# Kernel optimization log

Measured on AMD Instinct MI355X. Metric: run time of the kernel, lower is better.

## Reference

```python
import jax, jax.numpy as jnp
import numpy as np

E, K, B = 64, 8, 32
IN_DIM, OUT_DIM = 1024, 1024


def setup_inputs() -> dict:
    key = jax.random.key(0)
    k1, k2, k3, k4, k5, k6 = jax.random.split(key, 6)
    return {
        "weight_probs": jax.random.uniform(k1, (B, K), dtype=jnp.float32),
        "bias_probs": jax.random.uniform(k2, (B, K), dtype=jnp.float32),
        "weight_indices": jax.random.randint(k3, (B, K), 0, E, dtype=jnp.int64),
        "bias_indices": jax.random.randint(k4, (B, K), 0, E, dtype=jnp.int64),
        # parameter banks: one linear layer's params per expert
        "weight_bank": jax.random.normal(k5, (E, OUT_DIM, IN_DIM), dtype=jnp.float32) * 0.02,
        "bias_bank": jax.random.normal(k6, (E, OUT_DIM), dtype=jnp.float32) * 0.02,
    }


def reference(weight_probs, bias_probs, weight_indices, bias_indices, weight_bank, bias_bank):
    # _select_parameters: gather per-(batch, top_k) expert params
    sel_w = weight_bank[weight_indices]          # [B, K, O, I]
    sel_b = bias_bank[bias_indices]              # [B, K, O]
    # _compute_mixture: probability-weighted sum over the top_k axis
    weight_mixture = jnp.einsum("bk,bkoi->boi", weight_probs, sel_w)  # [B, O, I]
    bias_mixture = jnp.einsum("bk,bko->bo", bias_probs, sel_b)        # [B, O]
    return weight_mixture, bias_mixture
```

## Files before the change

kernel.cpp:

```cpp
#include <hip/hip_runtime.h>
#include <hip/hip_bf16.h>


typedef __attribute__((ext_vector_type(8)))  short short8v;
typedef __attribute__((ext_vector_type(16))) float f32x16;

constexpr int E = 64;
constexpr int K = 8;
constexpr int B = 32;
constexpr int IN_DIM = 1024;
constexpr int OUT_DIM = 1024;

constexpr int    NCOL     = OUT_DIM * IN_DIM;
constexpr int    BLK      = 256;
constexpr int    GRID     = 1024;
constexpr int    WAVES    = GRID * 4;
constexpr int    CGROUPS  = NCOL / 32;
constexpr int    STEPS    = CGROUPS / WAVES;
constexpr int    WM_ELEMS = B * NCOL;
constexpr int    OB4      = OUT_DIM / 4;
constexpr size_t WS_NEEDED = 2 * 4 * 64 * 8 * sizeof(short);

__global__ void ParameterMixture_build_afrag(
    const float* __restrict__ wprobs,
    const int*   __restrict__ widx,
    short*       __restrict__ afrag)
{
    const int t    = threadIdx.x;
    const int s    = t >> 6;
    const int lane = t & 63;
    const int m    = lane & 31;
    const int kh   = (lane >> 5) * 8;

#pragma unroll
    for (int j = 0; j < 8; ++j) {
        const int e = s * 16 + kh + j;
        float p = 0.f;
#pragma unroll
        for (int k2 = 0; k2 < K; ++k2)
            p += (widx[m * K + k2] == e) ? wprobs[m * K + k2] : 0.f;
        const __hip_bfloat16 h  = __float2bfloat16(p);
        const float          hf = __bfloat162float(h);
        const __hip_bfloat16 l  = __float2bfloat16(p - hf);
        afrag[(0 * 4 + s) * 512 + lane * 8 + j] = __builtin_bit_cast(short, h);
        afrag[(1 * 4 + s) * 512 + lane * 8 + j] = __builtin_bit_cast(short, l);
    }
}

__global__ __launch_bounds__(BLK, 4) void ParameterMixture_86835648790543_kernel(
    const float* __restrict__ wbank,
    const short* __restrict__ afrag,
    const float* __restrict__ bprobs,
    const int*   __restrict__ bidx,
    const float* __restrict__ bbank,
    float*       __restrict__ out)
{
    const int bid  = blockIdx.x;
    const int t    = threadIdx.x;
    const int wv   = t >> 6;
    const int lane = t & 63;

    if (bid < 32) {
        const int tt   = bid * BLK + t;
        const int b    = tt / OB4;
        const int off4 = tt % OB4;
        const float4* __restrict__ bb4 = (const float4*)bbank;
        float4 a4 = make_float4(0.f, 0.f, 0.f, 0.f);
#pragma unroll
        for (int k = 0; k < K; ++k) {
            const float p = bprobs[b * K + k];
            const int   e = bidx[b * K + k];
            const float4 v = bb4[e * OB4 + off4];
            a4.x += p * v.x; a4.y += p * v.y;
            a4.z += p * v.z; a4.w += p * v.w;
        }
        ((float4*)(out + WM_ELEMS))[tt] = a4;
    }

    short8v aH[4], aL[4];
#pragma unroll
    for (int s = 0; s < 4; ++s) {
        aH[s] = *(const short8v*)(afrag + s * 512 + lane * 8);
        aL[s] = *(const short8v*)(afrag + 2048 + s * 512 + lane * 8);
    }

    const int    cl   = lane & 31;
    const int    kh   = (lane >> 5) * 8;
    const size_t ncol = (size_t)NCOL;

    for (int step = 0; step < STEPS; ++step) {
        const int col0 = ((bid * 4 + wv) + step * WAVES) * 32;
        const float* __restrict__ wcol = wbank + col0 + cl;

        float w[4][8];
#pragma unroll
        for (int s = 0; s < 4; ++s)
#pragma unroll
            for (int j = 0; j < 8; ++j)
                w[s][j] = wcol[(size_t)(s * 16 + kh + j) * ncol];

        f32x16 acc;
#pragma unroll
        for (int i = 0; i < 16; ++i) acc[i] = 0.f;

#pragma unroll
        for (int s = 0; s < 4; ++s) {
            short8v bh, bl;
#pragma unroll
            for (int j = 0; j < 8; ++j) {
                const float x = w[s][j];
                const __hip_bfloat16 h  = __float2bfloat16(x);
                const float          hf = __bfloat162float(h);
                const __hip_bfloat16 l  = __float2bfloat16(x - hf);
                bh[j] = __builtin_bit_cast(short, h);
                bl[j] = __builtin_bit_cast(short, l);
            }
            acc = __builtin_amdgcn_mfma_f32_32x32x16_bf16(aH[s], bh, acc, 0, 0, 0);
            acc = __builtin_amdgcn_mfma_f32_32x32x16_bf16(aH[s], bl, acc, 0, 0, 0);
            acc = __builtin_amdgcn_mfma_f32_32x32x16_bf16(aL[s], bh, acc, 0, 0, 0);
        }

        float* __restrict__ ob = out + (size_t)((lane >> 5) * 4) * ncol + col0 + cl;
#pragma unroll
        for (int reg = 0; reg < 16; ++reg) {
            const int row = (reg & 3) + 8 * (reg >> 2);
            ob[(size_t)row * ncol] = acc[reg];
        }
    }
}

extern "C" void kernel_launch(void* const* d_in, const int* in_sizes, int n_in,
                              void* d_out, int out_size, void* d_ws, size_t ws_size,
                              hipStream_t stream) {
    const float* wprobs = (const float*)d_in[0];
    const float* bprobs = (const float*)d_in[1];
    const int*   widx   = (const int*)d_in[2];
    const int*   bidx   = (const int*)d_in[3];
    const float* wbank  = (const float*)d_in[4];
    const float* bbank  = (const float*)d_in[5];
    float*       out    = (float*)d_out;

    short* afrag = (short*)d_ws;

    ParameterMixture_build_afrag<<<1, BLK, 0, stream>>>(wprobs, widx, afrag);
    ParameterMixture_86835648790543_kernel<<<GRID, BLK, 0, stream>>>(
        wbank, afrag, bprobs, bidx, bbank, out);
}
```

Measured before the change: 93.83 us.

## Fuse A-fragment build into main kernel, contiguous column ranges, nontemporal stores

Drops the separate single-block kernel that built the bf16 hi/lo probability fragments. Each wave now rebuilds them in registers from the routing probabilities, which removes one launch and the dependency between kernels at the cost of redundant per-wave ALU work. Each wave now walks a contiguous range of columns instead of strided ones, and the loop is marked not to unroll. Output stores use nontemporal hints to avoid polluting the cache with the large write-once result.

```diff
diff --git a/kernel.cpp b/kernel.cpp
--- a/kernel.cpp
+++ b/kernel.cpp
@@ -11,47 +11,20 @@
 constexpr int IN_DIM = 1024;
 constexpr int OUT_DIM = 1024;
 
-constexpr int    NCOL     = OUT_DIM * IN_DIM;
-constexpr int    BLK      = 256;
-constexpr int    GRID     = 1024;
-constexpr int    WAVES    = GRID * 4;
-constexpr int    CGROUPS  = NCOL / 32;
-constexpr int    STEPS    = CGROUPS / WAVES;
-constexpr int    WM_ELEMS = B * NCOL;
-constexpr int    OB4      = OUT_DIM / 4;
-constexpr size_t WS_NEEDED = 2 * 4 * 64 * 8 * sizeof(short);
-
-__global__ void ParameterMixture_build_afrag(
-    const float* __restrict__ wprobs,
-    const int*   __restrict__ widx,
-    short*       __restrict__ afrag)
-{
-    const int t    = threadIdx.x;
-    const int s    = t >> 6;
-    const int lane = t & 63;
-    const int m    = lane & 31;
-    const int kh   = (lane >> 5) * 8;
-
-#pragma unroll
-    for (int j = 0; j < 8; ++j) {
-        const int e = s * 16 + kh + j;
-        float p = 0.f;
-#pragma unroll
-        for (int k2 = 0; k2 < K; ++k2)
-            p += (widx[m * K + k2] == e) ? wprobs[m * K + k2] : 0.f;
-        const __hip_bfloat16 h  = __float2bfloat16(p);
-        const float          hf = __bfloat162float(h);
-        const __hip_bfloat16 l  = __float2bfloat16(p - hf);
-        afrag[(0 * 4 + s) * 512 + lane * 8 + j] = __builtin_bit_cast(short, h);
-        afrag[(1 * 4 + s) * 512 + lane * 8 + j] = __builtin_bit_cast(short, l);
-    }
-}
+constexpr int NCOL     = OUT_DIM * IN_DIM;
+constexpr int BLK      = 256;
+constexpr int GRID     = 1024;
+constexpr int WAVES    = GRID * 4;
+constexpr int STEPS    = NCOL / 32 / WAVES;
+constexpr int WM_ELEMS = B * NCOL;
+constexpr int OB4      = OUT_DIM / 4;
 
 __global__ __launch_bounds__(BLK, 4) void ParameterMixture_86835648790543_kernel(
+    const float* __restrict__ wprobs,
+    const float* __restrict__ bprobs,
+    const int*   __restrict__ widx,
+    const int*   __restrict__ bidx,
     const float* __restrict__ wbank,
-    const short* __restrict__ afrag,
-    const float* __restrict__ bprobs,
-    const int*   __restrict__ bidx,
     const float* __restrict__ bbank,
     float*       __restrict__ out)
 {
@@ -59,6 +32,9 @@
     const int t    = threadIdx.x;
     const int wv   = t >> 6;
     const int lane = t & 63;
+    const int m    = lane & 31;
+    const int kh   = (lane >> 5) * 8;
+    const int cl   = lane & 31;
 
     if (bid < 32) {
         const int tt   = bid * BLK + t;
@@ -77,19 +53,37 @@
         ((float4*)(out + WM_ELEMS))[tt] = a4;
     }
 
+    float wp[K];
+    int   wi[K];
+#pragma unroll
+    for (int k2 = 0; k2 < K; ++k2) {
+        wp[k2] = wprobs[m * K + k2];
+        wi[k2] = widx[m * K + k2];
+    }
     short8v aH[4], aL[4];
 #pragma unroll
     for (int s = 0; s < 4; ++s) {
-        aH[s] = *(const short8v*)(afrag + s * 512 + lane * 8);
-        aL[s] = *(const short8v*)(afrag + 2048 + s * 512 + lane * 8);
+#pragma unroll
+        for (int j = 0; j < 8; ++j) {
+            const int e = s * 16 + kh + j;
+            float p = 0.f;
+#pragma unroll
+            for (int k2 = 0; k2 < K; ++k2)
+                p += (wi[k2] == e) ? wp[k2] : 0.f;
+            const __hip_bfloat16 h  = __float2bfloat16(p);
+            const float          hf = __bfloat162float(h);
+            const __hip_bfloat16 l  = __float2bfloat16(p - hf);
+            aH[s][j] = __builtin_bit_cast(short, h);
+            aL[s][j] = __builtin_bit_cast(short, l);
+        }
     }
 
-    const int    cl   = lane & 31;
-    const int    kh   = (lane >> 5) * 8;
-    const size_t ncol = (size_t)NCOL;
+    const size_t ncol    = (size_t)NCOL;
+    const int    wave_id = bid * 4 + wv;
 
+#pragma unroll 1
     for (int step = 0; step < STEPS; ++step) {
-        const int col0 = ((bid * 4 + wv) + step * WAVES) * 32;
+        const int col0 = wave_id * (32 * STEPS) + step * 32;
         const float* __restrict__ wcol = wbank + col0 + cl;
 
         float w[4][8];
@@ -124,7 +118,7 @@
 #pragma unroll
         for (int reg = 0; reg < 16; ++reg) {
             const int row = (reg & 3) + 8 * (reg >> 2);
-            ob[(size_t)row * ncol] = acc[reg];
+            __builtin_nontemporal_store(acc[reg], ob + (size_t)row * ncol);
         }
     }
 }
@@ -140,9 +134,6 @@
     const float* bbank  = (const float*)d_in[5];
     float*       out    = (float*)d_out;
 
-    short* afrag = (short*)d_ws;
-
-    ParameterMixture_build_afrag<<<1, BLK, 0, stream>>>(wprobs, widx, afrag);
     ParameterMixture_86835648790543_kernel<<<GRID, BLK, 0, stream>>>(
-        wbank, afrag, bprobs, bidx, bbank, out);
+        wprobs, bprobs, widx, bidx, wbank, bbank, out);
 }
```

Measured after the change: 96.15 us. +2.5%, slower.
